# Kernel optimization log

Measured on AMD Instinct MI355X. Metric: run time of the kernel, lower is better.

Reference implementation:

```python
import jax, jax.numpy as jnp
import numpy as np

STEP_SIZE = 0.005   # ray-march step length in normalized [-1,1] coords
RES = 128           # occupancy grid resolution per axis
NUM_BATCH = 4       # number of conditioned batches (B)
N_RAYS = 32768


def setup_inputs() -> dict:
    key = jax.random.key(0)
    k1, k2, k3, k4 = jax.random.split(key, 4)
    rays_o = jax.random.uniform(k1, (N_RAYS, 3), dtype=jnp.float32, minval=-0.5, maxval=0.5)
    d = jax.random.normal(k2, (N_RAYS, 3), dtype=jnp.float32)
    rays_d = d / jnp.linalg.norm(d, axis=-1, keepdims=True)
    rays_bidx = jax.random.randint(k3, (N_RAYS,), 0, NUM_BATCH)
    occ_grid = jax.random.uniform(k4, (NUM_BATCH, RES, RES, RES)) > 0.5
    return {"occ_grid": occ_grid, "rays_o": rays_o, "rays_d": rays_d,
            "rays_bidx": rays_bidx, "max_steps": 512}


def reference(occ_grid, rays_o, rays_d, rays_bidx, max_steps):
    """Batched occupancy-grid ray marching (uniform steps, dt_gamma=0, perturb=False).

    Returns:
      pts  [N, S, 3]: sample positions, zeroed where not occupied/out of range
      t    [N, S]   : per-step ray parameter
      mask [N, S]   : bool, sample is inside box AND its voxel is occupied
    """
    eps = 1e-10
    # --- ray / AABB([-1,1]^3) intersection -> near/far per ray ---
    safe_d = jnp.where(jnp.abs(rays_d) < eps,
                       jnp.where(rays_d >= 0, eps, -eps), rays_d)
    inv_d = 1.0 / safe_d
    t0 = (-1.0 - rays_o) * inv_d
    t1 = (1.0 - rays_o) * inv_d
    tmin = jnp.max(jnp.minimum(t0, t1), axis=-1)   # [N]
    tmax = jnp.min(jnp.maximum(t0, t1), axis=-1)   # [N]
    near = jnp.maximum(tmin, 0.0)

    # --- uniform marching: t_i = near + (i + 0.5) * step ---
    steps = jnp.arange(max_steps, dtype=rays_o.dtype)            # [S]
    t = near[:, None] + (steps + 0.5) * STEP_SIZE                # [N, S]
    pts = rays_o[:, None, :] + t[..., None] * rays_d[:, None, :]  # [N, S, 3]
    in_box = (t < tmax[:, None]) & (tmax > near)[:, None]        # [N, S]

    # --- occupancy query: gidx = clamp(((p/2+0.5)*R).long(), 0, R-1) ---
    gidx = jnp.clip(((pts * 0.5 + 0.5) * RES).astype(jnp.int32), 0, RES - 1)
    occ = occ_grid[rays_bidx[:, None], gidx[..., 0], gidx[..., 1], gidx[..., 2]]  # [N, S]
    mask = occ & in_box

    out_pts = pts * mask[..., None].astype(pts.dtype)
    return out_pts, t, mask
```

## Files before the change

### kernel.cpp

```cpp
#include <hip/hip_runtime.h>

constexpr int RESI   = 128;
constexpr int NSTEPS = 512;
constexpr int GRID_WORDS_PER_BATCH = 65536;

__global__ __launch_bounds__(256) void occ_pack_tiled_kernel(
    const int* __restrict__ occ, unsigned int* __restrict__ bits)
{
    const int w = blockIdx.x * blockDim.x + threadIdx.x;
    const int b   = w >> 16;
    const int rem = w & 65535;
    const int blockid = rem >> 4;
    const int wib     = rem & 15;
    const int bx = blockid >> 8;
    const int by = (blockid >> 4) & 15;
    const int bz = blockid & 15;
    const int gx  = bx * 8 + (wib >> 1);
    const int gy0 = by * 8 + (wib & 1) * 4;
    const int gz0 = bz * 8;

    const int* __restrict__ src = occ + (((size_t)b * RESI + gx) * RESI + gy0) * RESI + gz0;

    unsigned int word = 0;
#pragma unroll
    for (int a = 0; a < 4; ++a) {
        const int* row = src + a * RESI;
#pragma unroll
        for (int c = 0; c < 8; ++c) {
            const int v = __builtin_nontemporal_load(row + c);
            word |= (v != 0 ? 1u : 0u) << (a * 8 + c);
        }
    }
    bits[w] = word;
}

__global__ __launch_bounds__(256) void occ_march_kernel(
    const unsigned int* __restrict__ gridbits,
    const float* __restrict__ rays_o,
    const float* __restrict__ rays_d,
    const int*   __restrict__ rays_bidx,
    float*       __restrict__ out_pts,
    float*       __restrict__ out_t,
    float*       __restrict__ out_mask,
    int n_rays)
{
#pragma clang fp contract(off)
    const int n_pairs = n_rays >> 1;
    const int sub  = threadIdx.x >> 7;
    const int tid  = threadIdx.x & 127;
    const int s0   = tid * 4;

    for (int pair = blockIdx.x; pair < n_pairs; pair += gridDim.x) {
        const int ray = pair * 2 + sub;

        const float ox = rays_o[3 * ray + 0];
        const float oy = rays_o[3 * ray + 1];
        const float oz = rays_o[3 * ray + 2];
        const float dx = rays_d[3 * ray + 0];
        const float dy = rays_d[3 * ray + 1];
        const float dz = rays_d[3 * ray + 2];
        const int   b  = rays_bidx[ray];

        const float eps = 1e-10f;
        const float sdx = (fabsf(dx) < eps) ? ((dx >= 0.0f) ? eps : -eps) : dx;
        const float sdy = (fabsf(dy) < eps) ? ((dy >= 0.0f) ? eps : -eps) : dy;
        const float sdz = (fabsf(dz) < eps) ? ((dz >= 0.0f) ? eps : -eps) : dz;
        const float invx = 1.0f / sdx;
        const float invy = 1.0f / sdy;
        const float invz = 1.0f / sdz;

        const float t0x = (-1.0f - ox) * invx;
        const float t1x = ( 1.0f - ox) * invx;
        const float t0y = (-1.0f - oy) * invy;
        const float t1y = ( 1.0f - oy) * invy;
        const float t0z = (-1.0f - oz) * invz;
        const float t1z = ( 1.0f - oz) * invz;

        const float tmin = fmaxf(fmaxf(fminf(t0x, t1x), fminf(t0y, t1y)), fminf(t0z, t1z));
        const float tmax = fminf(fminf(fmaxf(t0x, t1x), fmaxf(t0y, t1y)), fmaxf(t0z, t1z));
        const float nearv  = fmaxf(tmin, 0.0f);
        const bool  ray_ok = (tmax > nearv);

        const unsigned int* __restrict__ gb = gridbits + (size_t)b * GRID_WORDS_PER_BATCH;

        float tv[4], px[4], py[4], pz[4];
        unsigned int widx[4], bitpos[4];
        bool in_box[4];

#pragma unroll
        for (int i = 0; i < 4; ++i) {
            const int s = s0 + i;
            const float ts = nearv + ((float)s + 0.5f) * 0.005f;
            const float x = ox + ts * dx;
            const float y = oy + ts * dy;
            const float z = oz + ts * dz;
            tv[i] = ts; px[i] = x; py[i] = y; pz[i] = z;
            in_box[i] = ray_ok && (ts < tmax);

            int gx = (int)((x * 0.5f + 0.5f) * 128.0f);
            int gy = (int)((y * 0.5f + 0.5f) * 128.0f);
            int gz = (int)((z * 0.5f + 0.5f) * 128.0f);
            gx = min(max(gx, 0), RESI - 1);
            gy = min(max(gy, 0), RESI - 1);
            gz = min(max(gz, 0), RESI - 1);

            const unsigned int blockid = ((unsigned)(gx >> 3) << 8) |
                                         ((unsigned)(gy >> 3) << 4) |
                                          (unsigned)(gz >> 3);
            const unsigned int wib = (((unsigned)gx & 7u) << 1) | (((unsigned)gy >> 2) & 1u);
            widx[i]   = (blockid << 4) | wib;
            bitpos[i] = (((unsigned)gy & 3u) << 3) | ((unsigned)gz & 7u);
        }

        unsigned int wrd[4];
#pragma unroll
        for (int i = 0; i < 4; ++i) wrd[i] = gb[widx[i]];

        float mv[4], p[12];
#pragma unroll
        for (int i = 0; i < 4; ++i) {
            const bool m = in_box[i] && ((wrd[i] >> bitpos[i]) & 1u);
            mv[i] = m ? 1.0f : 0.0f;
            p[3 * i + 0] = m ? px[i] : 0.0f;
            p[3 * i + 1] = m ? py[i] : 0.0f;
            p[3 * i + 2] = m ? pz[i] : 0.0f;
        }

        const size_t base = (size_t)ray * NSTEPS + (size_t)s0;

        *(float4*)(out_t    + base) = make_float4(tv[0], tv[1], tv[2], tv[3]);
        *(float4*)(out_mask + base) = make_float4(mv[0], mv[1], mv[2], mv[3]);

        float4* pp = (float4*)(out_pts + base * 3);
        pp[0] = make_float4(p[0], p[1], p[2],  p[3]);
        pp[1] = make_float4(p[4], p[5], p[6],  p[7]);
        pp[2] = make_float4(p[8], p[9], p[10], p[11]);
    }
}

extern "C" void kernel_launch(void* const* d_in, const int* in_sizes, int n_in,
                              void* d_out, int out_size, void* d_ws, size_t ws_size,
                              hipStream_t stream) {
    const int*   occ    = (const int*)  d_in[0];
    const float* rays_o = (const float*)d_in[1];
    const float* rays_d = (const float*)d_in[2];
    const int*   bidx   = (const int*)  d_in[3];

    const int n_rays = in_sizes[3];
    const int n_vox  = in_sizes[0];
    const int n_words = n_vox / 32;

    float* out      = (float*)d_out;
    float* out_pts  = out;
    float* out_t    = out + (size_t)n_rays * NSTEPS * 3;
    float* out_mask = out_t + (size_t)n_rays * NSTEPS;

    unsigned int* bits = (unsigned int*)d_ws;

    occ_pack_tiled_kernel<<<n_words / 256, 256, 0, stream>>>(occ, bits);
    occ_march_kernel<<<2048, 256, 0, stream>>>(bits, rays_o, rays_d, bidx,
                                               out_pts, out_t, out_mask, n_rays);
}
```

Measured before the change: 375.9 us.

## Stage point stores through swizzled LDS for coalesced writes, one ray per block

The march kernel now launches one 128-thread block per ray instead of a grid-stride loop over ray pairs. Each thread's 12 point floats are staged in shared memory using an XOR swizzle, so that after a barrier each wave writes its contiguous 3 KB slice of out_pts with lane-contiguous 16-byte stores rather than a 48-byte stride per lane. The aim is better store coalescing on the dominant output stream. In exchange it adds an LDS round trip, a block barrier, and launches many more small blocks.

Measured after the change: 366.9 us. 2.4% less time.

```diff
diff --git a/kernel.cpp b/kernel.cpp
--- a/kernel.cpp
+++ b/kernel.cpp
@@ -3,6 +3,8 @@
 constexpr int RESI   = 128;
 constexpr int NSTEPS = 512;
 constexpr int GRID_WORDS_PER_BATCH = 65536;
+
+typedef float v4f __attribute__((ext_vector_type(4)));
 
 __global__ __launch_bounds__(256) void occ_pack_tiled_kernel(
     const int* __restrict__ occ, unsigned int* __restrict__ bits)
@@ -34,7 +36,7 @@
     bits[w] = word;
 }
 
-__global__ __launch_bounds__(256) void occ_march_kernel(
+__global__ __launch_bounds__(128) void occ_march_kernel(
     const unsigned int* __restrict__ gridbits,
     const float* __restrict__ rays_o,
     const float* __restrict__ rays_d,
@@ -45,96 +47,112 @@
     int n_rays)
 {
 #pragma clang fp contract(off)
-    const int n_pairs = n_rays >> 1;
-    const int sub  = threadIdx.x >> 7;
-    const int tid  = threadIdx.x & 127;
+    __shared__ v4f sp[192 * 2];
+
+    const int ray = blockIdx.x;
+    if (ray >= n_rays) return;
+
+    const int tid  = threadIdx.x;
+    const int lane = tid & 63;
+    const int wv   = tid >> 6;
     const int s0   = tid * 4;
 
-    for (int pair = blockIdx.x; pair < n_pairs; pair += gridDim.x) {
-        const int ray = pair * 2 + sub;
+    const float ox = rays_o[3 * ray + 0];
+    const float oy = rays_o[3 * ray + 1];
+    const float oz = rays_o[3 * ray + 2];
+    const float dx = rays_d[3 * ray + 0];
+    const float dy = rays_d[3 * ray + 1];
+    const float dz = rays_d[3 * ray + 2];
+    const int   b  = rays_bidx[ray];
 
-        const float ox = rays_o[3 * ray + 0];
-        const float oy = rays_o[3 * ray + 1];
-        const float oz = rays_o[3 * ray + 2];
-        const float dx = rays_d[3 * ray + 0];
-        const float dy = rays_d[3 * ray + 1];
-        const float dz = rays_d[3 * ray + 2];
-        const int   b  = rays_bidx[ray];
+    const float eps = 1e-10f;
+    const float sdx = (fabsf(dx) < eps) ? ((dx >= 0.0f) ? eps : -eps) : dx;
+    const float sdy = (fabsf(dy) < eps) ? ((dy >= 0.0f) ? eps : -eps) : dy;
+    const float sdz = (fabsf(dz) < eps) ? ((dz >= 0.0f) ? eps : -eps) : dz;
+    const float invx = 1.0f / sdx;
+    const float invy = 1.0f / sdy;
+    const float invz = 1.0f / sdz;
 
-        const float eps = 1e-10f;
-        const float sdx = (fabsf(dx) < eps) ? ((dx >= 0.0f) ? eps : -eps) : dx;
-        const float sdy = (fabsf(dy) < eps) ? ((dy >= 0.0f) ? eps : -eps) : dy;
-        const float sdz = (fabsf(dz) < eps) ? ((dz >= 0.0f) ? eps : -eps) : dz;
-        const float invx = 1.0f / sdx;
-        const float invy = 1.0f / sdy;
-        const float invz = 1.0f / sdz;
+    const float t0x = (-1.0f - ox) * invx;
+    const float t1x = ( 1.0f - ox) * invx;
+    const float t0y = (-1.0f - oy) * invy;
+    const float t1y = ( 1.0f - oy) * invy;
+    const float t0z = (-1.0f - oz) * invz;
+    const float t1z = ( 1.0f - oz) * invz;
 
-        const float t0x = (-1.0f - ox) * invx;
-        const float t1x = ( 1.0f - ox) * invx;
-        const float t0y = (-1.0f - oy) * invy;
-        const float t1y = ( 1.0f - oy) * invy;
-        const float t0z = (-1.0f - oz) * invz;
-        const float t1z = ( 1.0f - oz) * invz;
+    const float tmin = fmaxf(fmaxf(fminf(t0x, t1x), fminf(t0y, t1y)), fminf(t0z, t1z));
+    const float tmax = fminf(fminf(fmaxf(t0x, t1x), fmaxf(t0y, t1y)), fmaxf(t0z, t1z));
+    const float nearv  = fmaxf(tmin, 0.0f);
+    const bool  ray_ok = (tmax > nearv);
 
-        const float tmin = fmaxf(fmaxf(fminf(t0x, t1x), fminf(t0y, t1y)), fminf(t0z, t1z));
-        const float tmax = fminf(fminf(fmaxf(t0x, t1x), fmaxf(t0y, t1y)), fmaxf(t0z, t1z));
-        const float nearv  = fmaxf(tmin, 0.0f);
-        const bool  ray_ok = (tmax > nearv);
+    const unsigned int* __restrict__ gb = gridbits + (size_t)b * GRID_WORDS_PER_BATCH;
 
-        const unsigned int* __restrict__ gb = gridbits + (size_t)b * GRID_WORDS_PER_BATCH;
-
-        float tv[4], px[4], py[4], pz[4];
-        unsigned int widx[4], bitpos[4];
-        bool in_box[4];
+    float tv[4], px[4], py[4], pz[4];
+    unsigned int widx[4], bitpos[4];
+    bool in_box[4];
 
 #pragma unroll
-        for (int i = 0; i < 4; ++i) {
-            const int s = s0 + i;
-            const float ts = nearv + ((float)s + 0.5f) * 0.005f;
-            const float x = ox + ts * dx;
-            const float y = oy + ts * dy;
-            const float z = oz + ts * dz;
-            tv[i] = ts; px[i] = x; py[i] = y; pz[i] = z;
-            in_box[i] = ray_ok && (ts < tmax);
+    for (int i = 0; i < 4; ++i) {
+        const int s = s0 + i;
+        const float ts = nearv + ((float)s + 0.5f) * 0.005f;
+        const float x = ox + ts * dx;
+        const float y = oy + ts * dy;
+        const float z = oz + ts * dz;
+        tv[i] = ts; px[i] = x; py[i] = y; pz[i] = z;
+        in_box[i] = ray_ok && (ts < tmax);
 
-            int gx = (int)((x * 0.5f + 0.5f) * 128.0f);
-            int gy = (int)((y * 0.5f + 0.5f) * 128.0f);
-            int gz = (int)((z * 0.5f + 0.5f) * 128.0f);
-            gx = min(max(gx, 0), RESI - 1);
-            gy = min(max(gy, 0), RESI - 1);
-            gz = min(max(gz, 0), RESI - 1);
+        int gx = (int)((x * 0.5f + 0.5f) * 128.0f);
+        int gy = (int)((y * 0.5f + 0.5f) * 128.0f);
+        int gz = (int)((z * 0.5f + 0.5f) * 128.0f);
+        gx = min(max(gx, 0), RESI - 1);
+        gy = min(max(gy, 0), RESI - 1);
+        gz = min(max(gz, 0), RESI - 1);
 
-            const unsigned int blockid = ((unsigned)(gx >> 3) << 8) |
-                                         ((unsigned)(gy >> 3) << 4) |
-                                          (unsigned)(gz >> 3);
-            const unsigned int wib = (((unsigned)gx & 7u) << 1) | (((unsigned)gy >> 2) & 1u);
-            widx[i]   = (blockid << 4) | wib;
-            bitpos[i] = (((unsigned)gy & 3u) << 3) | ((unsigned)gz & 7u);
-        }
+        const unsigned int blockid = ((unsigned)(gx >> 3) << 8) |
+                                     ((unsigned)(gy >> 3) << 4) |
+                                      (unsigned)(gz >> 3);
+        const unsigned int wib = (((unsigned)gx & 7u) << 1) | (((unsigned)gy >> 2) & 1u);
+        widx[i]   = (blockid << 4) | wib;
+        bitpos[i] = (((unsigned)gy & 3u) << 3) | ((unsigned)gz & 7u);
+    }
 
-        unsigned int wrd[4];
+    unsigned int wrd[4];
 #pragma unroll
-        for (int i = 0; i < 4; ++i) wrd[i] = gb[widx[i]];
+    for (int i = 0; i < 4; ++i) wrd[i] = gb[widx[i]];
 
-        float mv[4], p[12];
+    float mv[4], p[12];
 #pragma unroll
-        for (int i = 0; i < 4; ++i) {
-            const bool m = in_box[i] && ((wrd[i] >> bitpos[i]) & 1u);
-            mv[i] = m ? 1.0f : 0.0f;
-            p[3 * i + 0] = m ? px[i] : 0.0f;
-            p[3 * i + 1] = m ? py[i] : 0.0f;
-            p[3 * i + 2] = m ? pz[i] : 0.0f;
-        }
+    for (int i = 0; i < 4; ++i) {
+        const bool m = in_box[i] && ((wrd[i] >> bitpos[i]) & 1u);
+        mv[i] = m ? 1.0f : 0.0f;
+        p[3 * i + 0] = m ? px[i] : 0.0f;
+        p[3 * i + 1] = m ? py[i] : 0.0f;
+        p[3 * i + 2] = m ? pz[i] : 0.0f;
+    }
 
-        const size_t base = (size_t)ray * NSTEPS + (size_t)s0;
+    const size_t base = (size_t)ray * NSTEPS + (size_t)s0;
 
-        *(float4*)(out_t    + base) = make_float4(tv[0], tv[1], tv[2], tv[3]);
-        *(float4*)(out_mask + base) = make_float4(mv[0], mv[1], mv[2], mv[3]);
+    const v4f vt = { tv[0], tv[1], tv[2], tv[3] };
+    const v4f vm = { mv[0], mv[1], mv[2], mv[3] };
+    *(v4f*)(out_t    + base) = vt;
+    *(v4f*)(out_mask + base) = vm;
 
-        float4* pp = (float4*)(out_pts + base * 3);
-        pp[0] = make_float4(p[0], p[1], p[2],  p[3]);
-        pp[1] = make_float4(p[4], p[5], p[6],  p[7]);
-        pp[2] = make_float4(p[8], p[9], p[10], p[11]);
+    v4f* wbuf = sp + 192 * wv;
+#pragma unroll
+    for (int k = 0; k < 3; ++k) {
+        const int L = 3 * lane + k;
+        const int P = L ^ ((L >> 3) & 7);
+        wbuf[P] = (v4f){ p[4 * k + 0], p[4 * k + 1], p[4 * k + 2], p[4 * k + 3] };
+    }
+    __syncthreads();
+
+    float* ray_pts = out_pts + (size_t)ray * (NSTEPS * 3) + 768 * wv;
+#pragma unroll
+    for (int k = 0; k < 3; ++k) {
+        const int L = 64 * k + lane;
+        const int P = L ^ ((L >> 3) & 7);
+        const v4f v = wbuf[P];
+        *(v4f*)(ray_pts + 256 * k + 4 * lane) = v;
     }
 }
 
@@ -158,6 +176,6 @@
     unsigned int* bits = (unsigned int*)d_ws;
 
     occ_pack_tiled_kernel<<<n_words / 256, 256, 0, stream>>>(occ, bits);
-    occ_march_kernel<<<2048, 256, 0, stream>>>(bits, rays_o, rays_d, bidx,
-                                               out_pts, out_t, out_mask, n_rays);
+    occ_march_kernel<<<n_rays, 128, 0, stream>>>(bits, rays_o, rays_d, bidx,
+                                                 out_pts, out_t, out_mask, n_rays);
 }
```
